# Optimization experiments

Hardware: AMD Instinct MI355X
Metric: run time of the kernel (lower is better)

The kernel has to match this reference:

```python
import jax, jax.numpy as jnp
import numpy as np

N_NODES = 100000
N_FEATS = 256
OUT_DIM = 64
NNZ_X = 1280000
N_EDGES = 1600000
KEEP_PROB = 0.9  # 1 - dropout_rate (dropout_rate = 0.1)


def setup_inputs() -> dict:
    key = jax.random.key(0)
    ks = jax.random.split(key, 7)
    feat_values = jax.random.normal(ks[0], (NNZ_X,), dtype=jnp.float32)
    feat_rows = jax.random.randint(ks[1], (NNZ_X,), 0, N_NODES, dtype=jnp.int32)
    feat_cols = jax.random.randint(ks[2], (NNZ_X,), 0, N_FEATS, dtype=jnp.int32)
    # GlorotNormal kernel: std = sqrt(2 / (fan_in + fan_out))
    glorot_std = float(np.sqrt(2.0 / (N_FEATS + OUT_DIM)))
    kernel = jax.random.normal(ks[3], (N_FEATS, OUT_DIM), dtype=jnp.float32) * glorot_std
    adj_values = jax.random.uniform(ks[4], (N_EDGES,), dtype=jnp.float32)
    adj_rows = jax.random.randint(ks[5], (N_EDGES,), 0, N_NODES, dtype=jnp.int32)
    adj_cols = jax.random.randint(ks[6], (N_EDGES,), 0, N_NODES, dtype=jnp.int32)
    return {
        "feat_values": feat_values,
        "kernel": kernel,
        "adj_values": adj_values,
        "feat_rows": feat_rows,
        "feat_cols": feat_cols,
        "adj_rows": adj_rows,
        "adj_cols": adj_cols,
    }


def reference(feat_values, kernel, adj_values, feat_rows, feat_cols, adj_rows, adj_cols):
    # sparse dropout on feature values (training=True path), deterministic key.
    # tf: keep = floor(keep_prob + U[0,1)) cast to bool; retain then scale 1/keep_prob
    u = jax.random.uniform(jax.random.key(42), feat_values.shape, dtype=feat_values.dtype)
    keep = jnp.floor(KEEP_PROB + u).astype(bool)
    v = jnp.where(keep, feat_values, jnp.zeros_like(feat_values)) * (1.0 / KEEP_PROB)

    # SpMM 1: XW[n, o] = sum_{(n,f) in X} v * kernel[f, o]
    xw = jax.ops.segment_sum(v[:, None] * kernel[feat_cols], feat_rows,
                             num_segments=N_NODES)  # [N, OUT]

    # SpMM 2: out[i, o] = sum_{(i,j) in A} a_ij * xw[j, o]
    agg = jax.ops.segment_sum(adj_values[:, None] * xw[adj_cols], adj_rows,
                              num_segments=N_NODES)  # [N, OUT]

    return jax.nn.relu(agg)
```

## Files before the change

### kernel.cpp

```cpp
#include <hip/hip_runtime.h>

#define N_NODES 100000
#define N_FEATS 256
#define OUT_DIM 64
#define NNZ_X   1280000
#define N_EDGES 1600000
#define NB      391
#define CHUNK   4096
#define KPT     8
#define CAPX    4352
#define CAPA    5120
#define CAPXH   2560
#define CAPAH   3072

__device__ __forceinline__ unsigned rotl32(unsigned x, unsigned d) {
    return (x << d) | (x >> (32u - d));
}

__device__ __forceinline__ float jax_uniform_42(unsigned e) {
    unsigned x0 = 0u, x1 = e;
    const unsigned ks0 = 0u, ks1 = 42u, ks2 = 0u ^ 42u ^ 0x1BD11BDAu;
    x0 += ks0; x1 += ks1;
#define TF_R(r) { x0 += x1; x1 = rotl32(x1, r); x1 ^= x0; }
    TF_R(13) TF_R(15) TF_R(26) TF_R(6)
    x0 += ks1; x1 += ks2 + 1u;
    TF_R(17) TF_R(29) TF_R(16) TF_R(24)
    x0 += ks2; x1 += ks0 + 2u;
    TF_R(13) TF_R(15) TF_R(26) TF_R(6)
    x0 += ks0; x1 += ks1 + 3u;
    TF_R(17) TF_R(29) TF_R(16) TF_R(24)
    x0 += ks1; x1 += ks2 + 4u;
    TF_R(13) TF_R(15) TF_R(26) TF_R(6)
    x0 += ks2; x1 += ks0 + 5u;
#undef TF_R
    unsigned bits = x0 ^ x1;
    return __uint_as_float((bits >> 9) | 0x3f800000u) - 1.0f;
}

__device__ __forceinline__ bool keep_42(unsigned e) {
    float u = jax_uniform_42(e);
    return floorf(0.9f + u) != 0.0f;
}

__device__ __forceinline__ unsigned short f32_bf16(float f) {
    unsigned bits = __float_as_uint(f);
    return (unsigned short)((bits + 0x7fffu + ((bits >> 16) & 1u)) >> 16);
}

__device__ __forceinline__ float bflo(unsigned u) { return __uint_as_float(u << 16); }
__device__ __forceinline__ float bfhi(unsigned u) { return __uint_as_float(u & 0xffff0000u); }

__global__ __launch_bounds__(512) void phase1(
        const float* __restrict__ fvals, const int* __restrict__ frows,
        const int* __restrict__ fcols,
        const float* __restrict__ avals, const int* __restrict__ arows,
        const int* __restrict__ acols,
        int* __restrict__ bcur_x, int* __restrict__ bcur_a,
        float2* __restrict__ gx, float2* __restrict__ ga) {
    const int isA = blockIdx.y;
    const float* vals = isA ? avals : fvals;
    const int* rows   = isA ? arows : frows;
    const int* cols   = isA ? acols : fcols;
    int* bcur         = isA ? bcur_a : bcur_x;
    float2* dst       = isA ? ga : gx;
    const unsigned cap = isA ? CAPA : CAPX;
    const unsigned n  = isA ? N_EDGES : NNZ_X;

    unsigned t = threadIdx.x;
    unsigned base = blockIdx.x * CHUNK;
    if (base >= n) return;

    __shared__ int cnt[512];
    __shared__ int start[512];
    __shared__ int cur[512];
    __shared__ int gbase[NB];
    __shared__ int wtot[8];
    __shared__ int s_nvalid;
    __shared__ unsigned long long payload[CHUNK];
    __shared__ unsigned short bkt[CHUNK];

    int   rcache[KPT];
    float vcache[KPT];
    int   ccache[KPT];

    cnt[t] = 0;
    __syncthreads();
    #pragma unroll
    for (int k = 0; k < KPT; k++) {
        unsigned i = base + k * 512u + t;
        int r = -1;
        if (i < n) {
            int rr = rows[i];
            float v = vals[i];
            int   c = cols[i];
            if (isA || keep_42(i)) {
                r = rr;
                vcache[k] = isA ? v : v * (float)(1.0 / 0.9);
                ccache[k] = c;
            }
        }
        rcache[k] = r;
        if (r >= 0) atomicAdd(&cnt[(unsigned)r >> 8], 1);
    }
    __syncthreads();
    unsigned lane = t & 63u, wid = t >> 6;
    int binv = cnt[t];
    int inc = binv;
    #pragma unroll
    for (int d = 1; d < 64; d <<= 1) {
        int v = __shfl_up(inc, d, 64);
        if (lane >= (unsigned)d) inc += v;
    }
    if (lane == 63u) wtot[wid] = inc;
    __syncthreads();
    int offw = 0;
    #pragma unroll
    for (int w = 0; w < 8; w++) if ((unsigned)w < wid) offw += wtot[w];
    int excl = offw + inc - binv;
    start[t] = excl;
    cur[t]   = excl;
    if (t == 511u) s_nvalid = excl + binv;
    if (t < NB) {
        int cb = cnt[t];
        if (cb > 0) gbase[t] = atomicAdd(&bcur[t], cb);
    }
    __syncthreads();
    int n_valid = s_nvalid;
    #pragma unroll
    for (int k = 0; k < KPT; k++) {
        int r = rcache[k];
        if (r >= 0) {
            unsigned b = (unsigned)r >> 8;
            int p = atomicAdd(&cur[b], 1);
            unsigned packed = ((unsigned)ccache[k] << 8) | ((unsigned)r & 255u);
            payload[p] = ((unsigned long long)__float_as_uint(vcache[k]) << 32) | packed;
            bkt[p] = (unsigned short)b;
        }
    }
    __syncthreads();
    #pragma unroll
    for (int k = 0; k < KPT; k++) {
        int sidx = k * 512 + (int)t;
        if (sidx < n_valid) {
            unsigned b = bkt[sidx];
            unsigned long long m = payload[sidx];
            float2 e;
            e.x = __uint_as_float((unsigned)(m >> 32));
            e.y = __int_as_float((int)(unsigned)m);
            dst[(size_t)b * cap + gbase[b] + (sidx - start[b])] = e;
        }
    }
}

__global__ __launch_bounds__(512) void sort_x_spmm1(
        const int* __restrict__ bcur_x, const float2* __restrict__ gx,
        const float* __restrict__ W, unsigned short* __restrict__ xw) {
    __shared__ float2 ent[CAPXH];
    __shared__ int hist[128];
    __shared__ int starts[128];
    __shared__ int cursor[128];
    __shared__ int wtot[2];
    unsigned t = threadIdx.x;
    unsigned wid = t >> 6, lane = t & 63u;
    unsigned b = blockIdx.x >> 1, h = blockIdx.x & 1u;
    int cnt = bcur_x[b];
    const float2* src = gx + (size_t)b * CAPX;

    if (t < 128) hist[t] = 0;
    __syncthreads();
    float2 ec[9];
    unsigned mineMask = 0;
    #pragma unroll
    for (int k = 0; k < 9; k++) {
        int i = k * 512 + (int)t;
        if (i < cnt) {
            float2 e = src[i];
            ec[k] = e;
            unsigned pk = (unsigned)__float_as_int(e.y);
            if (((pk >> 7) & 1u) == h) {
                mineMask |= (1u << k);
                atomicAdd(&hist[pk & 127u], 1);
            }
        }
    }
    __syncthreads();
    int inc = 0, binv = 0;
    if (wid < 2u) {
        unsigned bin = wid * 64u + lane;
        binv = hist[bin];
        inc = binv;
        #pragma unroll
        for (int d = 1; d < 64; d <<= 1) {
            int v = __shfl_up(inc, d, 64);
            if (lane >= (unsigned)d) inc += v;
        }
        if (lane == 63u) wtot[wid] = inc;
    }
    __syncthreads();
    if (wid < 2u) {
        unsigned bin = wid * 64u + lane;
        int excl = inc - binv + (wid == 1u ? wtot[0] : 0);
        starts[bin] = excl;
        cursor[bin] = excl;
    }
    __syncthreads();
    #pragma unroll
    for (int k = 0; k < 9; k++) {
        if ((mineMask >> k) & 1u) {
            float2 e = ec[k];
            int pos = atomicAdd(&cursor[((unsigned)__float_as_int(e.y)) & 127u], 1);
            ent[pos] = e;
        }
    }
    __syncthreads();
    int cntH = wtot[0] + wtot[1];
    unsigned quarter = lane >> 4, sub = lane & 15u;
    const float4* W4 = (const float4*)W;
    ushort4* xw4 = (ushort4*)xw;
    for (unsigned r = wid; r < 128u; r += 8u) {
        int s0 = starts[r];
        int s1 = (r == 127u) ? cntH : starts[r + 1];
        float4 acc[4];
        #pragma unroll
        for (int j = 0; j < 4; j++) { acc[j].x = acc[j].y = acc[j].z = acc[j].w = 0.0f; }
        int p = s0;
        for (; p + 16 <= s1; p += 16) {
            float2 e[4];
            #pragma unroll
            for (int j = 0; j < 4; j++) e[j] = ent[p + 4 * quarter + j];
            float4 w[4];
            #pragma unroll
            for (int j = 0; j < 4; j++)
                w[j] = W4[(((unsigned)__float_as_int(e[j].y)) >> 8) * 16u + sub];
            #pragma unroll
            for (int j = 0; j < 4; j++) {
                acc[j].x = fmaf(e[j].x, w[j].x, acc[j].x);
                acc[j].y = fmaf(e[j].x, w[j].y, acc[j].y);
                acc[j].z = fmaf(e[j].x, w[j].z, acc[j].z);
                acc[j].w = fmaf(e[j].x, w[j].w, acc[j].w);
            }
        }
        for (int q = p + (int)quarter; q < s1; q += 4) {
            float2 e = ent[q];
            float4 w = W4[(((unsigned)__float_as_int(e.y)) >> 8) * 16u + sub];
            acc[0].x = fmaf(e.x, w.x, acc[0].x);
            acc[0].y = fmaf(e.x, w.y, acc[0].y);
            acc[0].z = fmaf(e.x, w.z, acc[0].z);
            acc[0].w = fmaf(e.x, w.w, acc[0].w);
        }
        float ax = (acc[0].x + acc[1].x) + (acc[2].x + acc[3].x);
        float ay = (acc[0].y + acc[1].y) + (acc[2].y + acc[3].y);
        float az = (acc[0].z + acc[1].z) + (acc[2].z + acc[3].z);
        float aw = (acc[0].w + acc[1].w) + (acc[2].w + acc[3].w);
        ax += __shfl(ax, (int)(lane ^ 16u), 64);
        ay += __shfl(ay, (int)(lane ^ 16u), 64);
        az += __shfl(az, (int)(lane ^ 16u), 64);
        aw += __shfl(aw, (int)(lane ^ 16u), 64);
        ax += __shfl(ax, (int)(lane ^ 32u), 64);
        ay += __shfl(ay, (int)(lane ^ 32u), 64);
        az += __shfl(az, (int)(lane ^ 32u), 64);
        aw += __shfl(aw, (int)(lane ^ 32u), 64);
        unsigned grow = (b << 8) + (h << 7) + r;
        if (quarter == 0 && grow < N_NODES) {
            ushort4 o;
            o.x = f32_bf16(ax); o.y = f32_bf16(ay);
            o.z = f32_bf16(az); o.w = f32_bf16(aw);
            xw4[(size_t)grow * 16u + sub] = o;
        }
    }
}

__global__ __launch_bounds__(512) void sort_a_spmm2(
        const int* __restrict__ bcur_a, const float2* __restrict__ ga,
        const unsigned short* __restrict__ xw, float* __restrict__ out) {
    __shared__ float2 ent[CAPAH];
    __shared__ int hist[128];
    __shared__ int starts[128];
    __shared__ int cursor[128];
    __shared__ int wtot[2];
    unsigned t = threadIdx.x;
    unsigned wid = t >> 6, lane = t & 63u;
    unsigned b = blockIdx.x >> 1, h = blockIdx.x & 1u;
    int cnt = bcur_a[b];
    const float2* src = ga + (size_t)b * CAPA;

    if (t < 128) hist[t] = 0;
    __syncthreads();
    float2 ec[10];
    unsigned mineMask = 0;
    #pragma unroll
    for (int k = 0; k < 10; k++) {
        int i = k * 512 + (int)t;
        if (i < cnt) {
            float2 e = src[i];
            ec[k] = e;
            unsigned pk = (unsigned)__float_as_int(e.y);
            if (((pk >> 7) & 1u) == h) {
                mineMask |= (1u << k);
                atomicAdd(&hist[pk & 127u], 1);
            }
        }
    }
    __syncthreads();
    int inc = 0, binv = 0;
    if (wid < 2u) {
        unsigned bin = wid * 64u + lane;
        binv = hist[bin];
        inc = binv;
        #pragma unroll
        for (int d = 1; d < 64; d <<= 1) {
            int v = __shfl_up(inc, d, 64);
            if (lane >= (unsigned)d) inc += v;
        }
        if (lane == 63u) wtot[wid] = inc;
    }
    __syncthreads();
    if (wid < 2u) {
        unsigned bin = wid * 64u + lane;
        int excl = inc - binv + (wid == 1u ? wtot[0] : 0);
        starts[bin] = excl;
        cursor[bin] = excl;
    }
    __syncthreads();
    #pragma unroll
    for (int k = 0; k < 10; k++) {
        if ((mineMask >> k) & 1u) {
            float2 e = ec[k];
            int pos = atomicAdd(&cursor[((unsigned)__float_as_int(e.y)) & 127u], 1);
            ent[pos] = e;
        }
    }
    __syncthreads();
    int cntH = wtot[0] + wtot[1];
    unsigned oct = lane >> 3, sub = lane & 7u;
    const uint4* xw8 = (const uint4*)xw;
    for (unsigned r = wid; r < 128u; r += 8u) {
        int s0 = starts[r];
        int s1 = (r == 127u) ? cntH : starts[r + 1];
        float acc[8];
        #pragma unroll
        for (int j = 0; j < 8; j++) acc[j] = 0.0f;
        int p = s0 + (int)oct;
        for (; p + 8 < s1; p += 16) {
            float2 e0 = ent[p];
            float2 e1 = ent[p + 8];
            uint4 u0 = xw8[(((unsigned)__float_as_int(e0.y)) >> 8) * 8u + sub];
            uint4 u1 = xw8[(((unsigned)__float_as_int(e1.y)) >> 8) * 8u + sub];
            float v0 = e0.x, v1 = e1.x;
            acc[0] = fmaf(v0, bflo(u0.x), acc[0]);
            acc[1] = fmaf(v0, bfhi(u0.x), acc[1]);
            acc[2] = fmaf(v0, bflo(u0.y), acc[2]);
            acc[3] = fmaf(v0, bfhi(u0.y), acc[3]);
            acc[4] = fmaf(v0, bflo(u0.z), acc[4]);
            acc[5] = fmaf(v0, bfhi(u0.z), acc[5]);
            acc[6] = fmaf(v0, bflo(u0.w), acc[6]);
            acc[7] = fmaf(v0, bfhi(u0.w), acc[7]);
            acc[0] = fmaf(v1, bflo(u1.x), acc[0]);
            acc[1] = fmaf(v1, bfhi(u1.x), acc[1]);
            acc[2] = fmaf(v1, bflo(u1.y), acc[2]);
            acc[3] = fmaf(v1, bfhi(u1.y), acc[3]);
            acc[4] = fmaf(v1, bflo(u1.z), acc[4]);
            acc[5] = fmaf(v1, bfhi(u1.z), acc[5]);
            acc[6] = fmaf(v1, bflo(u1.w), acc[6]);
            acc[7] = fmaf(v1, bfhi(u1.w), acc[7]);
        }
        if (p < s1) {
            float2 e = ent[p];
            uint4 u = xw8[(((unsigned)__float_as_int(e.y)) >> 8) * 8u + sub];
            float v = e.x;
            acc[0] = fmaf(v, bflo(u.x), acc[0]);
            acc[1] = fmaf(v, bfhi(u.x), acc[1]);
            acc[2] = fmaf(v, bflo(u.y), acc[2]);
            acc[3] = fmaf(v, bfhi(u.y), acc[3]);
            acc[4] = fmaf(v, bflo(u.z), acc[4]);
            acc[5] = fmaf(v, bfhi(u.z), acc[5]);
            acc[6] = fmaf(v, bflo(u.w), acc[6]);
            acc[7] = fmaf(v, bfhi(u.w), acc[7]);
        }
        #pragma unroll
        for (int j = 0; j < 8; j++) {
            acc[j] += __shfl_xor(acc[j], 8, 64);
            acc[j] += __shfl_xor(acc[j], 16, 64);
            acc[j] += __shfl_xor(acc[j], 32, 64);
        }
        unsigned grow = (b << 8) + (h << 7) + r;
        if (oct == 0 && grow < N_NODES) {
            float4 o0, o1;
            o0.x = fmaxf(acc[0], 0.0f);
            o0.y = fmaxf(acc[1], 0.0f);
            o0.z = fmaxf(acc[2], 0.0f);
            o0.w = fmaxf(acc[3], 0.0f);
            o1.x = fmaxf(acc[4], 0.0f);
            o1.y = fmaxf(acc[5], 0.0f);
            o1.z = fmaxf(acc[6], 0.0f);
            o1.w = fmaxf(acc[7], 0.0f);
            float4* op = (float4*)(out + (size_t)grow * 64u + sub * 8u);
            op[0] = o0;
            op[1] = o1;
        }
    }
}

extern "C" void kernel_launch(void* const* d_in, const int* in_sizes, int n_in,
                              void* d_out, int out_size, void* d_ws, size_t ws_size,
                              hipStream_t stream) {
    const float* feat_values = (const float*)d_in[0];
    const float* W           = (const float*)d_in[1];
    const float* adj_values  = (const float*)d_in[2];
    const int*   feat_rows   = (const int*)d_in[3];
    const int*   feat_cols   = (const int*)d_in[4];
    const int*   adj_rows    = (const int*)d_in[5];
    const int*   adj_cols    = (const int*)d_in[6];
    float* out = (float*)d_out;

    char* ws = (char*)d_ws;
    int* bcur_x = (int*)(ws + 0);
    int* bcur_a = (int*)(ws + 2048);
    float2* gx  = (float2*)(ws + 204800);
    float2* ga  = (float2*)(ws + 13817856);
    unsigned short* xw = (unsigned short*)(ws + 29833216);

    hipMemsetAsync(ws, 0, 4096, stream);

    dim3 gp1((N_EDGES + CHUNK - 1) / CHUNK, 2);
    phase1<<<gp1, 512, 0, stream>>>(feat_values, feat_rows, feat_cols,
                                    adj_values, adj_rows, adj_cols,
                                    bcur_x, bcur_a, gx, ga);
    sort_x_spmm1<<<2 * NB, 512, 0, stream>>>(bcur_x, gx, W, xw);
    sort_a_spmm2<<<2 * NB, 512, 0, stream>>>(bcur_a, ga, xw, out);
}
```

Before: 181.1 us.

## Bucket edges by 128-row groups in phase1 so later kernels skip half-filtering

The first pass now bins nonzeros into 782 buckets of 128 rows instead of 391 buckets of 256 rows. Each block of the two SpMM kernels reads only its own half-sized bucket, no longer loading and discarding the other half. This removes redundant global reads and masking in the sort kernels. In exchange phase1 carries a larger shared histogram, scatters into more global buckets with more atomics, and has smaller per-bucket capacities that may overflow under skewed inputs.

```diff
diff --git a/kernel.cpp b/kernel.cpp
--- a/kernel.cpp
+++ b/kernel.cpp
@@ -5,11 +5,9 @@
 #define OUT_DIM 64
 #define NNZ_X   1280000
 #define N_EDGES 1600000
-#define NB      391
+#define NBH     782
 #define CHUNK   4096
 #define KPT     8
-#define CAPX    4352
-#define CAPA    5120
 #define CAPXH   2560
 #define CAPAH   3072
 
@@ -63,17 +61,16 @@
     const int* cols   = isA ? acols : fcols;
     int* bcur         = isA ? bcur_a : bcur_x;
     float2* dst       = isA ? ga : gx;
-    const unsigned cap = isA ? CAPA : CAPX;
+    const unsigned cap = isA ? CAPAH : CAPXH;
     const unsigned n  = isA ? N_EDGES : NNZ_X;
 
     unsigned t = threadIdx.x;
     unsigned base = blockIdx.x * CHUNK;
     if (base >= n) return;
 
-    __shared__ int cnt[512];
-    __shared__ int start[512];
-    __shared__ int cur[512];
-    __shared__ int gbase[NB];
+    __shared__ int cnt[1024];
+    __shared__ int start[1024];
+    __shared__ int gofs[NBH];
     __shared__ int wtot[8];
     __shared__ int s_nvalid;
     __shared__ unsigned long long payload[CHUNK];
@@ -84,6 +81,7 @@
     int   ccache[KPT];
 
     cnt[t] = 0;
+    cnt[t + 512] = 0;
     __syncthreads();
     #pragma unroll
     for (int k = 0; k < KPT; k++) {
@@ -100,12 +98,13 @@
             }
         }
         rcache[k] = r;
-        if (r >= 0) atomicAdd(&cnt[(unsigned)r >> 8], 1);
+        if (r >= 0) atomicAdd(&cnt[(unsigned)r >> 7], 1);
     }
     __syncthreads();
     unsigned lane = t & 63u, wid = t >> 6;
-    int binv = cnt[t];
-    int inc = binv;
+    int c0 = cnt[2 * t], c1 = cnt[2 * t + 1];
+    int pairsum = c0 + c1;
+    int inc = pairsum;
     #pragma unroll
     for (int d = 1; d < 64; d <<= 1) {
         int v = __shfl_up(inc, d, 64);
@@ -116,13 +115,17 @@
     int offw = 0;
     #pragma unroll
     for (int w = 0; w < 8; w++) if ((unsigned)w < wid) offw += wtot[w];
-    int excl = offw + inc - binv;
-    start[t] = excl;
-    cur[t]   = excl;
-    if (t == 511u) s_nvalid = excl + binv;
-    if (t < NB) {
-        int cb = cnt[t];
-        if (cb > 0) gbase[t] = atomicAdd(&bcur[t], cb);
+    int excl = offw + inc - pairsum;
+    start[2 * t]     = excl;
+    start[2 * t + 1] = excl + c0;
+    if (t == 511u) s_nvalid = excl + pairsum;
+    __syncthreads();
+    for (unsigned bb = t; bb < NBH; bb += 512u) {
+        int cb = cnt[bb];
+        if (cb > 0) {
+            int g = atomicAdd(&bcur[bb], cb);
+            gofs[bb] = g - start[bb];
+        }
     }
     __syncthreads();
     int n_valid = s_nvalid;
@@ -130,9 +133,9 @@
     for (int k = 0; k < KPT; k++) {
         int r = rcache[k];
         if (r >= 0) {
-            unsigned b = (unsigned)r >> 8;
-            int p = atomicAdd(&cur[b], 1);
-            unsigned packed = ((unsigned)ccache[k] << 8) | ((unsigned)r & 255u);
+            unsigned b = (unsigned)r >> 7;
+            int p = atomicAdd(&start[b], 1);
+            unsigned packed = ((unsigned)ccache[k] << 7) | ((unsigned)r & 127u);
             payload[p] = ((unsigned long long)__float_as_uint(vcache[k]) << 32) | packed;
             bkt[p] = (unsigned short)b;
         }
@@ -147,7 +150,7 @@
             float2 e;
             e.x = __uint_as_float((unsigned)(m >> 32));
             e.y = __int_as_float((int)(unsigned)m);
-            dst[(size_t)b * cap + gbase[b] + (sidx - start[b])] = e;
+            dst[(size_t)b * cap + gofs[b] + sidx] = e;
         }
     }
 }
@@ -162,25 +165,20 @@
     __shared__ int wtot[2];
     unsigned t = threadIdx.x;
     unsigned wid = t >> 6, lane = t & 63u;
-    unsigned b = blockIdx.x >> 1, h = blockIdx.x & 1u;
+    unsigned b = blockIdx.x;
     int cnt = bcur_x[b];
-    const float2* src = gx + (size_t)b * CAPX;
+    const float2* src = gx + (size_t)b * CAPXH;
 
     if (t < 128) hist[t] = 0;
     __syncthreads();
-    float2 ec[9];
-    unsigned mineMask = 0;
-    #pragma unroll
-    for (int k = 0; k < 9; k++) {
+    float2 ec[5];
+    #pragma unroll
+    for (int k = 0; k < 5; k++) {
         int i = k * 512 + (int)t;
         if (i < cnt) {
             float2 e = src[i];
             ec[k] = e;
-            unsigned pk = (unsigned)__float_as_int(e.y);
-            if (((pk >> 7) & 1u) == h) {
-                mineMask |= (1u << k);
-                atomicAdd(&hist[pk & 127u], 1);
-            }
+            atomicAdd(&hist[((unsigned)__float_as_int(e.y)) & 127u], 1);
         }
     }
     __syncthreads();
@@ -205,21 +203,21 @@
     }
     __syncthreads();
     #pragma unroll
-    for (int k = 0; k < 9; k++) {
-        if ((mineMask >> k) & 1u) {
+    for (int k = 0; k < 5; k++) {
+        int i = k * 512 + (int)t;
+        if (i < cnt) {
             float2 e = ec[k];
             int pos = atomicAdd(&cursor[((unsigned)__float_as_int(e.y)) & 127u], 1);
             ent[pos] = e;
         }
     }
     __syncthreads();
-    int cntH = wtot[0] + wtot[1];
     unsigned quarter = lane >> 4, sub = lane & 15u;
     const float4* W4 = (const float4*)W;
     ushort4* xw4 = (ushort4*)xw;
     for (unsigned r = wid; r < 128u; r += 8u) {
         int s0 = starts[r];
-        int s1 = (r == 127u) ? cntH : starts[r + 1];
+        int s1 = (r == 127u) ? cnt : starts[r + 1];
         float4 acc[4];
         #pragma unroll
         for (int j = 0; j < 4; j++) { acc[j].x = acc[j].y = acc[j].z = acc[j].w = 0.0f; }
@@ -231,7 +229,7 @@
             float4 w[4];
             #pragma unroll
             for (int j = 0; j < 4; j++)
-                w[j] = W4[(((unsigned)__float_as_int(e[j].y)) >> 8) * 16u + sub];
+                w[j] = W4[(((unsigned)__float_as_int(e[j].y)) >> 7) * 16u + sub];
             #pragma unroll
             for (int j = 0; j < 4; j++) {
                 acc[j].x = fmaf(e[j].x, w[j].x, acc[j].x);
@@ -242,7 +240,7 @@
         }
         for (int q = p + (int)quarter; q < s1; q += 4) {
             float2 e = ent[q];
-            float4 w = W4[(((unsigned)__float_as_int(e.y)) >> 8) * 16u + sub];
+            float4 w = W4[(((unsigned)__float_as_int(e.y)) >> 7) * 16u + sub];
             acc[0].x = fmaf(e.x, w.x, acc[0].x);
             acc[0].y = fmaf(e.x, w.y, acc[0].y);
             acc[0].z = fmaf(e.x, w.z, acc[0].z);
@@ -260,7 +258,7 @@
         ay += __shfl(ay, (int)(lane ^ 32u), 64);
         az += __shfl(az, (int)(lane ^ 32u), 64);
         aw += __shfl(aw, (int)(lane ^ 32u), 64);
-        unsigned grow = (b << 8) + (h << 7) + r;
+        unsigned grow = (b << 7) + r;
         if (quarter == 0 && grow < N_NODES) {
             ushort4 o;
             o.x = f32_bf16(ax); o.y = f32_bf16(ay);
@@ -280,25 +278,20 @@
     __shared__ int wtot[2];
     unsigned t = threadIdx.x;
     unsigned wid = t >> 6, lane = t & 63u;
-    unsigned b = blockIdx.x >> 1, h = blockIdx.x & 1u;
+    unsigned b = blockIdx.x;
     int cnt = bcur_a[b];
-    const float2* src = ga + (size_t)b * CAPA;
+    const float2* src = ga + (size_t)b * CAPAH;
 
     if (t < 128) hist[t] = 0;
     __syncthreads();
-    float2 ec[10];
-    unsigned mineMask = 0;
-    #pragma unroll
-    for (int k = 0; k < 10; k++) {
+    float2 ec[6];
+    #pragma unroll
+    for (int k = 0; k < 6; k++) {
         int i = k * 512 + (int)t;
         if (i < cnt) {
             float2 e = src[i];
             ec[k] = e;
-            unsigned pk = (unsigned)__float_as_int(e.y);
-            if (((pk >> 7) & 1u) == h) {
-                mineMask |= (1u << k);
-                atomicAdd(&hist[pk & 127u], 1);
-            }
+            atomicAdd(&hist[((unsigned)__float_as_int(e.y)) & 127u], 1);
         }
     }
     __syncthreads();
@@ -323,20 +316,20 @@
     }
     __syncthreads();
     #pragma unroll
-    for (int k = 0; k < 10; k++) {
-        if ((mineMask >> k) & 1u) {
+    for (int k = 0; k < 6; k++) {
+        int i = k * 512 + (int)t;
+        if (i < cnt) {
             float2 e = ec[k];
             int pos = atomicAdd(&cursor[((unsigned)__float_as_int(e.y)) & 127u], 1);
             ent[pos] = e;
         }
     }
     __syncthreads();
-    int cntH = wtot[0] + wtot[1];
     unsigned oct = lane >> 3, sub = lane & 7u;
     const uint4* xw8 = (const uint4*)xw;
     for (unsigned r = wid; r < 128u; r += 8u) {
         int s0 = starts[r];
-        int s1 = (r == 127u) ? cntH : starts[r + 1];
+        int s1 = (r == 127u) ? cnt : starts[r + 1];
         float acc[8];
         #pragma unroll
         for (int j = 0; j < 8; j++) acc[j] = 0.0f;
@@ -344,8 +337,8 @@
         for (; p + 8 < s1; p += 16) {
             float2 e0 = ent[p];
             float2 e1 = ent[p + 8];
-            uint4 u0 = xw8[(((unsigned)__float_as_int(e0.y)) >> 8) * 8u + sub];
-            uint4 u1 = xw8[(((unsigned)__float_as_int(e1.y)) >> 8) * 8u + sub];
+            uint4 u0 = xw8[(((unsigned)__float_as_int(e0.y)) >> 7) * 8u + sub];
+            uint4 u1 = xw8[(((unsigned)__float_as_int(e1.y)) >> 7) * 8u + sub];
             float v0 = e0.x, v1 = e1.x;
             acc[0] = fmaf(v0, bflo(u0.x), acc[0]);
             acc[1] = fmaf(v0, bfhi(u0.x), acc[1]);
@@ -366,7 +359,7 @@
         }
         if (p < s1) {
             float2 e = ent[p];
-            uint4 u = xw8[(((unsigned)__float_as_int(e.y)) >> 8) * 8u + sub];
+            uint4 u = xw8[(((unsigned)__float_as_int(e.y)) >> 7) * 8u + sub];
             float v = e.x;
             acc[0] = fmaf(v, bflo(u.x), acc[0]);
             acc[1] = fmaf(v, bfhi(u.x), acc[1]);
@@ -383,7 +376,7 @@
             acc[j] += __shfl_xor(acc[j], 16, 64);
             acc[j] += __shfl_xor(acc[j], 32, 64);
         }
-        unsigned grow = (b << 8) + (h << 7) + r;
+        unsigned grow = (b << 7) + r;
         if (oct == 0 && grow < N_NODES) {
             float4 o0, o1;
             o0.x = fmaxf(acc[0], 0.0f);
@@ -415,17 +408,17 @@
 
     char* ws = (char*)d_ws;
     int* bcur_x = (int*)(ws + 0);
-    int* bcur_a = (int*)(ws + 2048);
-    float2* gx  = (float2*)(ws + 204800);
-    float2* ga  = (float2*)(ws + 13817856);
-    unsigned short* xw = (unsigned short*)(ws + 29833216);
-
-    hipMemsetAsync(ws, 0, 4096, stream);
+    int* bcur_a = (int*)(ws + 4096);
+    float2* gx  = (float2*)(ws + 16384);
+    float2* ga  = (float2*)(ws + 16384 + 16015360);
+    unsigned short* xw = (unsigned short*)(ws + 35250176);
+
+    hipMemsetAsync(ws, 0, 8192, stream);
 
     dim3 gp1((N_EDGES + CHUNK - 1) / CHUNK, 2);
     phase1<<<gp1, 512, 0, stream>>>(feat_values, feat_rows, feat_cols,
                                     adj_values, adj_rows, adj_cols,
                                     bcur_x, bcur_a, gx, ga);
-    sort_x_spmm1<<<2 * NB, 512, 0, stream>>>(bcur_x, gx, W, xw);
-    sort_a_spmm2<<<2 * NB, 512, 0, stream>>>(bcur_a, ga, xw, out);
-}
+    sort_x_spmm1<<<NBH, 512, 0, stream>>>(bcur_x, gx, W, xw);
+    sort_a_spmm2<<<NBH, 512, 0, stream>>>(bcur_a, ga, xw, out);
+}
```

New measurement: 181.2 us. About the same (+0.0%).
